# Performance work log

Hardware: AMD Instinct MI355X
Metric: run time of the kernel (lower is better)

## Reference

```python
import jax, jax.numpy as jnp
import numpy as np

B, T, D_IN, D, N = 8, 1024, 512, 512, 64

def setup_inputs() -> dict:
    key = jax.random.key(0)
    ks = jax.random.split(key, 8)
    s = 0.02  # weight init scale keeps tanh/softmax in sane range
    return {
        'x': jax.random.normal(ks[0], (B, T, D_IN), jnp.float32),
        'h_tape_init': jax.random.normal(ks[1], (B, N, D), jnp.float32),
        'h_work_init': jax.random.normal(ks[2], (B, D), jnp.float32) * 0.1,
        'W_h': jax.random.normal(ks[3], (D, D), jnp.float32) * s,
        'W_xz': jax.random.normal(ks[4], (2 * D, D_IN), jnp.float32) * s,
        'b_h': jnp.zeros((D,), jnp.float32),
        'W_write': jax.random.normal(ks[5], (D, D), jnp.float32) * s,
        'g_z': jnp.ones((D,), jnp.float32),
        'g_r': jnp.ones((D,), jnp.float32),
        'g_h': jnp.ones((D,), jnp.float32),
        'b_gate': jnp.zeros((D,), jnp.float32),
    }

def reference(x, h_tape_init, h_work_init, W_h, W_xz, b_h, W_write, g_z, g_r, g_h, b_gate):
    d = W_h.shape[0]
    scale = 1.0 / np.sqrt(d).astype(np.float32)
    xz = jnp.einsum('btk,ek->bte', x, W_xz)          # [B,T,2D]
    x_proj = xz[..., :d]
    z = xz[..., d:]

    def step(carry, inp):
        h_tape, h_work = carry                        # [B,N,D], [B,D]
        x_t, z_t = inp                                # [B,D], [B,D]
        read_scores = jnp.einsum('bd,bnd->bn', h_work, h_tape) * scale
        read_attn = jax.nn.softmax(read_scores, axis=-1)
        read_val = jnp.einsum('bn,bnd->bd', read_attn, h_tape)
        h_new = jnp.tanh(x_t + h_work @ W_h.T + read_val + b_h)
        write_val = h_new @ W_write.T
        write_scores = jnp.einsum('bd,bnd->bn', write_val, h_tape) * scale
        write_attn = jax.nn.softmax(write_scores, axis=-1)[..., None]  # [B,N,1]
        h_tape_new = h_tape * (1.0 - write_attn) + write_val[:, None, :] * write_attn
        gate_in = jnp.clip(z_t * g_z + read_val * g_r + h_new * g_h + b_gate, -20.0, 20.0)
        out = h_new * jax.nn.silu(gate_in)
        return (h_tape_new, h_new), out

    (h_tape_final, _), outs = jax.lax.scan(
        step, (h_tape_init, h_work_init),
        (jnp.swapaxes(x_proj, 0, 1), jnp.swapaxes(z, 0, 1)))
    return jnp.swapaxes(outs, 0, 1), h_tape_final
```

## Files before the change

### kernel.cpp

```cpp
#include <hip/hip_runtime.h>
#include <math.h>

#define TT 1024
#define DD 512

typedef unsigned int u32;
typedef unsigned long long u64;
typedef _Float16 half2_t __attribute__((ext_vector_type(2)));

static __device__ __forceinline__ u64 aload64(const u64* p) {
    return __hip_atomic_load(p, __ATOMIC_RELAXED, __HIP_MEMORY_SCOPE_AGENT);
}
static __device__ __forceinline__ void astore64(u64* p, u64 v) {
    __hip_atomic_store(p, v, __ATOMIC_RELAXED, __HIP_MEMORY_SCOPE_AGENT);
}
static __device__ __forceinline__ u32 pkh2(float lo, float hi) {
    return __builtin_bit_cast(u32, __builtin_amdgcn_cvt_pkrtz(lo, hi));
}
static __device__ __forceinline__ float2 uph2(u32 v) {
    half2_t h = __builtin_bit_cast(half2_t, v);
    return make_float2((float)h.x, (float)h.y);
}
static __device__ __forceinline__ u64 mkword(u32 pay, u32 tag) {
    return ((u64)tag << 32) | (u64)pay;
}

static __device__ __forceinline__ float redux8(float v) {
    v += __shfl_xor(v, 1); v += __shfl_xor(v, 2); v += __shfl_xor(v, 4); return v;
}
static __device__ __forceinline__ float sum64(float v) {
    #pragma unroll
    for (int o = 32; o > 0; o >>= 1) v += __shfl_xor(v, o);
    return v;
}
static __device__ __forceinline__ float expc(float x) { return __expf(fminf(x, 60.f)); }
static __device__ __forceinline__ float fast_tanh(float x) {
    float xc = fminf(fmaxf(x, -15.f), 15.f);
    float e = __expf(2.f * xc);
    return (e - 1.f) / (e + 1.f);
}

__global__ __launch_bounds__(256) void proj_kernel(const float* __restrict__ x,
                                                   const float* __restrict__ Wxz,
                                                   float* __restrict__ xp,
                                                   float* __restrict__ z) {
    __shared__ float As[16][66];
    __shared__ float Bs[16][66];
    const int m0 = blockIdx.x * 64;
    const int n0 = blockIdx.y * 64;
    const int tid = threadIdx.x;
    const int tm = tid / 16, tn = tid % 16;
    float c[4][4] = {};
    for (int k0 = 0; k0 < 512; k0 += 16) {
        const int r = tid >> 2, c4 = (tid & 3) * 4;
        float4 a4 = *(const float4*)(x + (size_t)(m0 + r) * 512 + k0 + c4);
        float4 b4 = *(const float4*)(Wxz + (size_t)(n0 + r) * 512 + k0 + c4);
        As[c4 + 0][r] = a4.x; As[c4 + 1][r] = a4.y; As[c4 + 2][r] = a4.z; As[c4 + 3][r] = a4.w;
        Bs[c4 + 0][r] = b4.x; Bs[c4 + 1][r] = b4.y; Bs[c4 + 2][r] = b4.z; Bs[c4 + 3][r] = b4.w;
        __syncthreads();
        #pragma unroll
        for (int k = 0; k < 16; ++k) {
            float a0 = As[k][tm * 4 + 0], a1 = As[k][tm * 4 + 1];
            float a2 = As[k][tm * 4 + 2], a3 = As[k][tm * 4 + 3];
            float b0 = Bs[k][tn * 4 + 0], b1 = Bs[k][tn * 4 + 1];
            float b2 = Bs[k][tn * 4 + 2], b3 = Bs[k][tn * 4 + 3];
            c[0][0] += a0 * b0; c[0][1] += a0 * b1; c[0][2] += a0 * b2; c[0][3] += a0 * b3;
            c[1][0] += a1 * b0; c[1][1] += a1 * b1; c[1][2] += a1 * b2; c[1][3] += a1 * b3;
            c[2][0] += a2 * b0; c[2][1] += a2 * b1; c[2][2] += a2 * b2; c[2][3] += a2 * b3;
            c[3][0] += a3 * b0; c[3][1] += a3 * b1; c[3][2] += a3 * b2; c[3][3] += a3 * b3;
        }
        __syncthreads();
    }
    #pragma unroll
    for (int i = 0; i < 4; ++i) {
        const int m = m0 + tm * 4 + i;
        #pragma unroll
        for (int j = 0; j < 4; ++j) {
            const int e = n0 + tn * 4 + j;
            if (e < 512) xp[(size_t)m * 512 + e] = c[i][j];
            else         z[(size_t)m * 512 + (e - 512)] = c[i][j];
        }
    }
}

__global__ __launch_bounds__(512) void rec_kernel(
    const float* __restrict__ tape0, const float* __restrict__ hwork0,
    const float* __restrict__ W_h, const float* __restrict__ b_h,
    const float* __restrict__ W_write,
    const float* __restrict__ g_z, const float* __restrict__ g_r,
    const float* __restrict__ g_h, const float* __restrict__ b_gate,
    const float* __restrict__ Zbuf,
    float* __restrict__ out, float* __restrict__ tape_out,
    u64* hA, u64* cA) {
    __shared__ __align__(16) float tp[64][512];
    __shared__ __align__(16) float hw2[8][68];
    __shared__ __align__(16) float wvp[8][68];
    __shared__ float red[8][64];
    __shared__ __align__(16) float hnc[64];
    __shared__ float rvc[64], xpc[64], zc[64];
    __shared__ float a_l[64], c1_l[64], hhc[64], ws_l[64], q0_l[64];
    __shared__ float c2_s;

    const int b = blockIdx.x & 7, s = blockIdx.x >> 3;
    const int tid = threadIdx.x, lane = tid & 63, wid = tid >> 6;
    const int nrow = tid >> 3, l = tid & 7;
    const int sw = ((l ^ nrow) & 7) << 2;
    const int d0 = s * 64;
    const float scale = 0.044194173824159216f;

    float4 wh[16];
    float4 wwc[16];
    {
        const float4* w1 = (const float4*)(W_h + (size_t)(d0 + nrow) * DD + l * 64);
        #pragma unroll
        for (int j = 0; j < 16; ++j) wh[j] = w1[j];
        const float4* w2 = (const float4*)(W_write + (size_t)tid * DD + d0);
        #pragma unroll
        for (int j = 0; j < 16; ++j) wwc[j] = w2[j];
    }
    float bhr = 0.f, gz = 0.f, gr = 0.f, gh = 0.f, bg = 0.f;
    if (wid == 0) bhr = b_h[d0 + lane];
    if (wid == 1) { gz = g_z[d0 + lane]; gr = g_r[d0 + lane]; gh = g_h[d0 + lane]; bg = b_gate[d0 + lane]; }

    {
        const float* src = tape0 + (size_t)(b * 64 + nrow) * DD;
        #pragma unroll
        for (int i = 0; i < 16; ++i) {
            float4 v = *(const float4*)(src + l * 64 + 4 * i);
            *(float4*)&tp[nrow][(l * 64 + 4 * i) ^ sw] = v;
        }
    }
    hw2[tid >> 6][tid & 63] = hwork0[(size_t)b * DD + tid];
    {
        float* pw = &wvp[0][0];
        for (int i = tid; i < 8 * 68; i += 512) pw[i] = 0.f;
    }
    if (tid < 64) a_l[tid] = 0.f;
    if (tid == 0) c2_s = 0.f;
    float xpr = 0.f, zr = 0.f;
    if (wid == 2)      xpr = out[((size_t)(b * TT)) * DD + d0 + lane];
    else if (wid == 3) zr  = Zbuf[((size_t)(b * TT)) * DD + d0 + lane];
    __syncthreads();

    {
        float q0 = 0.f, hh = 0.f;
        #pragma unroll
        for (int i = 0; i < 16; ++i) {
            float4 t4 = *(const float4*)&tp[nrow][(l * 64 + 4 * i) ^ sw];
            float4 h4 = *(const float4*)&hw2[l][4 * i];
            q0 += t4.x * h4.x + t4.y * h4.y + t4.z * h4.z + t4.w * h4.w;
            hh += wh[i].x * h4.x + wh[i].y * h4.y + wh[i].z * h4.z + wh[i].w * h4.w;
        }
        q0 = redux8(q0); hh = redux8(hh);
        if (l == 0) { q0_l[nrow] = q0; hhc[nrow] = hh; }
    }
    __syncthreads();
    if (wid == 0) {
        float er = expc(scale * q0_l[lane]);
        float Zr = sum64(er);
        c1_l[lane] = __fdividef(er, Zr);
    }
    __syncthreads();

    for (int t = 0; t < TT; ++t) {
        const int p = t & 1;
        const u32 tg = (u32)(t + 1);

        if (wid == 2)      xpc[lane] = xpr;
        else if (wid == 3) zc[lane] = zr;
        {
            float acc = 0.f;
            #pragma unroll
            for (int k = 0; k < 8; ++k)
                acc += c1_l[wid * 8 + k] * tp[wid * 8 + k][(d0 + lane) ^ (((s ^ k) & 7) << 2)];
            red[wid][lane] = acc;
        }
        __syncthreads();
        if (wid == 0) {
            float rv = c2_s * wvp[s][lane];
            #pragma unroll
            for (int w = 0; w < 8; ++w) rv += red[w][lane];
            rvc[lane] = rv;
            hnc[lane] = fast_tanh(xpc[lane] + hhc[lane] + rv + bhr);
        }
        __syncthreads();
        if (wid == 0 && !(lane & 1))
            astore64(&hA[((size_t)p * 8 + b) * 256 + s * 32 + (lane >> 1)],
                     mkword(pkh2(hnc[lane], hnc[lane + 1]), tg));
        {
            float cj = 0.f;
            #pragma unroll
            for (int j = 0; j < 16; ++j) {
                float4 h4 = *(const float4*)&hnc[4 * j];
                cj += wwc[j].x * h4.x + wwc[j].y * h4.y + wwc[j].z * h4.z + wwc[j].w * h4.w;
            }
            float cn = __shfl_xor(cj, 1);
            if (!(tid & 1))
                astore64(&cA[(((size_t)p * 8 + b) * 8 + s) * 256 + (tid >> 1)],
                         mkword(pkh2(cj, cn), tg));
        }
        if (wid == 1) {
            float h = hnc[lane];
            float g = zc[lane] * gz + rvc[lane] * gr + h * gh + bg;
            g = fminf(fmaxf(g, -20.f), 20.f);
            float sig = 1.f / (1.f + __expf(-g));
            out[((size_t)(b * TT + t)) * DD + d0 + lane] = h * g * sig;
        }
        const float an = a_l[nrow];
        #pragma unroll
        for (int i = 0; i < 8; ++i) {
            const int c = (l * 64 + 4 * i) ^ sw;
            float4 t4 = *(const float4*)&tp[nrow][c];
            float4 w4 = *(const float4*)&wvp[l][4 * i];
            t4.x += an * (w4.x - t4.x); t4.y += an * (w4.y - t4.y);
            t4.z += an * (w4.z - t4.z); t4.w += an * (w4.w - t4.w);
            *(float4*)&tp[nrow][c] = t4;
        }
        u64 v0 = 0, v1 = 0, v2 = 0, v3 = 0, v4 = 0, v5 = 0, v6 = 0, v7 = 0, vhw = 0;
        if (tid < 256) {
            const u64* cb = cA + (((size_t)p * 8 + b) * 8) * 256 + tid;
            v0 = aload64(cb + 0 * 256); v1 = aload64(cb + 1 * 256);
            v2 = aload64(cb + 2 * 256); v3 = aload64(cb + 3 * 256);
            v4 = aload64(cb + 4 * 256); v5 = aload64(cb + 5 * 256);
            v6 = aload64(cb + 6 * 256); v7 = aload64(cb + 7 * 256);
        } else {
            vhw = aload64(hA + ((size_t)p * 8 + b) * 256 + (tid - 256));
        }
        #pragma unroll
        for (int i = 8; i < 16; ++i) {
            const int c = (l * 64 + 4 * i) ^ sw;
            float4 t4 = *(const float4*)&tp[nrow][c];
            float4 w4 = *(const float4*)&wvp[l][4 * i];
            t4.x += an * (w4.x - t4.x); t4.y += an * (w4.y - t4.y);
            t4.z += an * (w4.z - t4.z); t4.w += an * (w4.w - t4.w);
            *(float4*)&tp[nrow][c] = t4;
        }
        __syncthreads();
        if (tid < 256) {
            const u64* cb = cA + (((size_t)p * 8 + b) * 8) * 256 + tid;
            for (;;) {
                u32 m = 0;
                if ((u32)(v0 >> 32) == tg) m |= 1u;   if ((u32)(v1 >> 32) == tg) m |= 2u;
                if ((u32)(v2 >> 32) == tg) m |= 4u;   if ((u32)(v3 >> 32) == tg) m |= 8u;
                if ((u32)(v4 >> 32) == tg) m |= 16u;  if ((u32)(v5 >> 32) == tg) m |= 32u;
                if ((u32)(v6 >> 32) == tg) m |= 64u;  if ((u32)(v7 >> 32) == tg) m |= 128u;
                if (m == 0xffu) break;
                __builtin_amdgcn_s_sleep(1);
                if (!(m & 1u))   v0 = aload64(cb + 0 * 256);
                if (!(m & 2u))   v1 = aload64(cb + 1 * 256);
                if (!(m & 4u))   v2 = aload64(cb + 2 * 256);
                if (!(m & 8u))   v3 = aload64(cb + 3 * 256);
                if (!(m & 16u))  v4 = aload64(cb + 4 * 256);
                if (!(m & 32u))  v5 = aload64(cb + 5 * 256);
                if (!(m & 64u))  v6 = aload64(cb + 6 * 256);
                if (!(m & 128u)) v7 = aload64(cb + 7 * 256);
            }
            float lo = 0.f, hi = 0.f; float2 f;
            f = uph2((u32)v0); lo += f.x; hi += f.y;
            f = uph2((u32)v1); lo += f.x; hi += f.y;
            f = uph2((u32)v2); lo += f.x; hi += f.y;
            f = uph2((u32)v3); lo += f.x; hi += f.y;
            f = uph2((u32)v4); lo += f.x; hi += f.y;
            f = uph2((u32)v5); lo += f.x; hi += f.y;
            f = uph2((u32)v6); lo += f.x; hi += f.y;
            f = uph2((u32)v7); lo += f.x; hi += f.y;
            wvp[tid >> 5][2 * (tid & 31)]     = lo;
            wvp[tid >> 5][2 * (tid & 31) + 1] = hi;
        } else {
            const int k = tid - 256;
            const u64* hb = hA + ((size_t)p * 8 + b) * 256 + k;
            for (;;) {
                if ((u32)(vhw >> 32) == tg) break;
                __builtin_amdgcn_s_sleep(1);
                vhw = aload64(hb);
            }
            float2 hp = uph2((u32)vhw);
            hw2[k >> 5][2 * (k & 31)]     = hp.x;
            hw2[k >> 5][2 * (k & 31) + 1] = hp.y;
        }
        __syncthreads();
        float hwv = 0.f;
        {
            float ws = 0.f, q0 = 0.f, hh = 0.f;
            #pragma unroll
            for (int i = 0; i < 16; ++i) {
                float4 t4 = *(const float4*)&tp[nrow][(l * 64 + 4 * i) ^ sw];
                float4 w4 = *(const float4*)&wvp[l][4 * i];
                float4 h4 = *(const float4*)&hw2[l][4 * i];
                ws += w4.x * t4.x + w4.y * t4.y + w4.z * t4.z + w4.w * t4.w;
                q0 += h4.x * t4.x + h4.y * t4.y + h4.z * t4.z + h4.w * t4.w;
                hh += wh[i].x * h4.x + wh[i].y * h4.y + wh[i].z * h4.z + wh[i].w * h4.w;
            }
            ws = redux8(ws); q0 = redux8(q0); hh = redux8(hh);
            if (l == 0) { ws_l[nrow] = ws; q0_l[nrow] = q0; hhc[nrow] = hh; }
        }
        if (wid == 0) {
            const int r8 = lane >> 3, c8 = (lane & 7) * 8;
            float a = 0.f;
            #pragma unroll
            for (int k = 0; k < 8; ++k) a += hw2[r8][c8 + k] * wvp[r8][c8 + k];
            hwv = sum64(a);
        }
        if (wid == 2 && t + 1 < TT)      xpr = out[((size_t)(b * TT + t + 1)) * DD + d0 + lane];
        else if (wid == 3 && t + 1 < TT) zr  = Zbuf[((size_t)(b * TT + t + 1)) * DD + d0 + lane];
        __syncthreads();
        if (wid == 0) {
            float ew = expc(scale * ws_l[lane]);
            float Zw = sum64(ew);
            float a = __fdividef(ew, Zw);
            float q = (1.f - a) * q0_l[lane] + a * hwv;
            float er = expc(scale * q);
            float Zr = sum64(er);
            float r = __fdividef(er, Zr);
            a_l[lane] = a;
            c1_l[lane] = r * (1.f - a);
            float c2 = sum64(r * a);
            if (lane == 0) c2_s = c2;
        }
        __syncthreads();
    }

    {
        const float an = a_l[nrow];
        const int esw = ((s ^ nrow) & 7) << 2;
        float* dst = tape_out + ((size_t)(b * 64 + nrow)) * DD;
        #pragma unroll
        for (int i = 0; i < 2; ++i) {
            const int c0 = d0 + l * 8 + 4 * i;
            float4 t4 = *(const float4*)&tp[nrow][c0 ^ esw];
            float4 w4 = *(const float4*)&wvp[s][l * 8 + 4 * i];
            t4.x += an * (w4.x - t4.x); t4.y += an * (w4.y - t4.y);
            t4.z += an * (w4.z - t4.z); t4.w += an * (w4.w - t4.w);
            *(float4*)(dst + c0) = t4;
        }
    }
}

extern "C" void kernel_launch(void* const* d_in, const int* in_sizes, int n_in,
                              void* d_out, int out_size, void* d_ws, size_t ws_size,
                              hipStream_t stream) {
    const float* x       = (const float*)d_in[0];
    const float* tape0   = (const float*)d_in[1];
    const float* hwork0  = (const float*)d_in[2];
    const float* W_h     = (const float*)d_in[3];
    const float* W_xz    = (const float*)d_in[4];
    const float* b_h     = (const float*)d_in[5];
    const float* W_write = (const float*)d_in[6];
    const float* g_z     = (const float*)d_in[7];
    const float* g_r     = (const float*)d_in[8];
    const float* g_h     = (const float*)d_in[9];
    const float* b_gate  = (const float*)d_in[10];

    float* out  = (float*)d_out;
    float* tout = out + (size_t)8 * TT * DD;

    char* ws = (char*)d_ws;
    u64* hA   = (u64*)ws;
    u64* cA   = (u64*)(ws + 32768);
    float* Zbuf = (float*)(ws + 393216);

    (void)in_sizes; (void)n_in; (void)out_size; (void)ws_size;

    dim3 pgrid(128, 16);
    proj_kernel<<<pgrid, 256, 0, stream>>>(x, W_xz, out, Zbuf);
    rec_kernel<<<64, 512, 0, stream>>>(tape0, hwork0, W_h, b_h, W_write,
                                       g_z, g_r, g_h, b_gate, Zbuf,
                                       out, tout, hA, cA);
}
```

Baseline: 4.977 ms.

## Cut per-step barriers by fusing read_val/tanh into softmax warp and double-buffering write values

Moves the read-value reduction and tanh into wave 0 right after the softmax, so h_new is ready at the end of each step and two block barriers per timestep disappear. The write-value buffer is double-buffered by step parity so the tape update can run before the new write values are published without a separate barrier, and updated tape rows are kept in registers for the following score dot products instead of being re-read from LDS. The trade-off is that a single wave now does the 64-row read_val loop serially, which lengthens the critical path and raises register pressure (launch bounds also ask for two blocks per CU).

```diff
diff --git a/kernel.cpp b/kernel.cpp
--- a/kernel.cpp
+++ b/kernel.cpp
@@ -83,7 +83,7 @@
     }
 }
 
-__global__ __launch_bounds__(512) void rec_kernel(
+__global__ __launch_bounds__(512, 2) void rec_kernel(
     const float* __restrict__ tape0, const float* __restrict__ hwork0,
     const float* __restrict__ W_h, const float* __restrict__ b_h,
     const float* __restrict__ W_write,
@@ -94,12 +94,12 @@
     u64* hA, u64* cA) {
     __shared__ __align__(16) float tp[64][512];
     __shared__ __align__(16) float hw2[8][68];
-    __shared__ __align__(16) float wvp[8][68];
-    __shared__ float red[8][64];
+    __shared__ __align__(16) float wvp[2][8][68];
     __shared__ __align__(16) float hnc[64];
-    __shared__ float rvc[64], xpc[64], zc[64];
-    __shared__ float a_l[64], c1_l[64], hhc[64], ws_l[64], q0_l[64];
-    __shared__ float c2_s;
+    __shared__ float rvc[64];
+    __shared__ float a_l[64], c1_l[64];
+    __shared__ float ws_l[64], q0_l[64], hhc[64];
+    __shared__ float hwv_s;
 
     const int b = blockIdx.x & 7, s = blockIdx.x >> 3;
     const int tid = threadIdx.x, lane = tid & 63, wid = tid >> 6;
@@ -132,14 +132,13 @@
     }
     hw2[tid >> 6][tid & 63] = hwork0[(size_t)b * DD + tid];
     {
-        float* pw = &wvp[0][0];
-        for (int i = tid; i < 8 * 68; i += 512) pw[i] = 0.f;
+        float* pw = &wvp[0][0][0];
+        for (int i = tid; i < 2 * 8 * 68; i += 512) pw[i] = 0.f;
     }
     if (tid < 64) a_l[tid] = 0.f;
-    if (tid == 0) c2_s = 0.f;
-    float xpr = 0.f, zr = 0.f;
-    if (wid == 2)      xpr = out[((size_t)(b * TT)) * DD + d0 + lane];
-    else if (wid == 3) zr  = Zbuf[((size_t)(b * TT)) * DD + d0 + lane];
+    float xpr = 0.f, zr = 0.f, hr = 0.f;
+    if (wid == 0)      xpr = out[((size_t)(b * TT)) * DD + d0 + lane];
+    else if (wid == 1) zr  = Zbuf[((size_t)(b * TT)) * DD + d0 + lane];
     __syncthreads();
 
     {
@@ -158,7 +157,14 @@
     if (wid == 0) {
         float er = expc(scale * q0_l[lane]);
         float Zr = sum64(er);
-        c1_l[lane] = __fdividef(er, Zr);
+        float r = __fdividef(er, Zr);
+        c1_l[lane] = r;
+        float rv = 0.f;
+        #pragma unroll 8
+        for (int n = 0; n < 64; ++n)
+            rv += c1_l[n] * tp[n][(d0 + lane) ^ (((s ^ n) & 7) << 2)];
+        float h = fast_tanh(xpr + hhc[lane] + rv + bhr);
+        hr = h; hnc[lane] = h; rvc[lane] = rv;
     }
     __syncthreads();
 
@@ -166,27 +172,12 @@
         const int p = t & 1;
         const u32 tg = (u32)(t + 1);
 
-        if (wid == 2)      xpc[lane] = xpr;
-        else if (wid == 3) zc[lane] = zr;
-        {
-            float acc = 0.f;
-            #pragma unroll
-            for (int k = 0; k < 8; ++k)
-                acc += c1_l[wid * 8 + k] * tp[wid * 8 + k][(d0 + lane) ^ (((s ^ k) & 7) << 2)];
-            red[wid][lane] = acc;
-        }
-        __syncthreads();
         if (wid == 0) {
-            float rv = c2_s * wvp[s][lane];
-            #pragma unroll
-            for (int w = 0; w < 8; ++w) rv += red[w][lane];
-            rvc[lane] = rv;
-            hnc[lane] = fast_tanh(xpc[lane] + hhc[lane] + rv + bhr);
-        }
-        __syncthreads();
-        if (wid == 0 && !(lane & 1))
-            astore64(&hA[((size_t)p * 8 + b) * 256 + s * 32 + (lane >> 1)],
-                     mkword(pkh2(hnc[lane], hnc[lane + 1]), tg));
+            float hn = __shfl_xor(hr, 1);
+            if (!(lane & 1))
+                astore64(&hA[((size_t)p * 8 + b) * 256 + s * 32 + (lane >> 1)],
+                         mkword(pkh2(hr, hn), tg));
+        }
         {
             float cj = 0.f;
             #pragma unroll
@@ -201,43 +192,33 @@
         }
         if (wid == 1) {
             float h = hnc[lane];
-            float g = zc[lane] * gz + rvc[lane] * gr + h * gh + bg;
+            float g = zr * gz + rvc[lane] * gr + h * gh + bg;
             g = fminf(fmaxf(g, -20.f), 20.f);
             float sig = 1.f / (1.f + __expf(-g));
             out[((size_t)(b * TT + t)) * DD + d0 + lane] = h * g * sig;
-        }
+            if (t + 1 < TT) zr = Zbuf[((size_t)(b * TT + t + 1)) * DD + d0 + lane];
+        }
+        if (wid == 0 && t + 1 < TT) xpr = out[((size_t)(b * TT + t + 1)) * DD + d0 + lane];
+
         const float an = a_l[nrow];
-        #pragma unroll
-        for (int i = 0; i < 8; ++i) {
+        float4 t4[16];
+        #pragma unroll
+        for (int i = 0; i < 16; ++i) {
             const int c = (l * 64 + 4 * i) ^ sw;
-            float4 t4 = *(const float4*)&tp[nrow][c];
-            float4 w4 = *(const float4*)&wvp[l][4 * i];
-            t4.x += an * (w4.x - t4.x); t4.y += an * (w4.y - t4.y);
-            t4.z += an * (w4.z - t4.z); t4.w += an * (w4.w - t4.w);
-            *(float4*)&tp[nrow][c] = t4;
-        }
-        u64 v0 = 0, v1 = 0, v2 = 0, v3 = 0, v4 = 0, v5 = 0, v6 = 0, v7 = 0, vhw = 0;
+            float4 v = *(const float4*)&tp[nrow][c];
+            float4 w4 = *(const float4*)&wvp[1 - p][l][4 * i];
+            v.x += an * (w4.x - v.x); v.y += an * (w4.y - v.y);
+            v.z += an * (w4.z - v.z); v.w += an * (w4.w - v.w);
+            *(float4*)&tp[nrow][c] = v;
+            t4[i] = v;
+        }
+
         if (tid < 256) {
             const u64* cb = cA + (((size_t)p * 8 + b) * 8) * 256 + tid;
-            v0 = aload64(cb + 0 * 256); v1 = aload64(cb + 1 * 256);
-            v2 = aload64(cb + 2 * 256); v3 = aload64(cb + 3 * 256);
-            v4 = aload64(cb + 4 * 256); v5 = aload64(cb + 5 * 256);
-            v6 = aload64(cb + 6 * 256); v7 = aload64(cb + 7 * 256);
-        } else {
-            vhw = aload64(hA + ((size_t)p * 8 + b) * 256 + (tid - 256));
-        }
-        #pragma unroll
-        for (int i = 8; i < 16; ++i) {
-            const int c = (l * 64 + 4 * i) ^ sw;
-            float4 t4 = *(const float4*)&tp[nrow][c];
-            float4 w4 = *(const float4*)&wvp[l][4 * i];
-            t4.x += an * (w4.x - t4.x); t4.y += an * (w4.y - t4.y);
-            t4.z += an * (w4.z - t4.z); t4.w += an * (w4.w - t4.w);
-            *(float4*)&tp[nrow][c] = t4;
-        }
-        __syncthreads();
-        if (tid < 256) {
-            const u64* cb = cA + (((size_t)p * 8 + b) * 8) * 256 + tid;
+            u64 v0 = aload64(cb + 0 * 256), v1 = aload64(cb + 1 * 256);
+            u64 v2 = aload64(cb + 2 * 256), v3 = aload64(cb + 3 * 256);
+            u64 v4 = aload64(cb + 4 * 256), v5 = aload64(cb + 5 * 256);
+            u64 v6 = aload64(cb + 6 * 256), v7 = aload64(cb + 7 * 256);
             for (;;) {
                 u32 m = 0;
                 if ((u32)(v0 >> 32) == tg) m |= 1u;   if ((u32)(v1 >> 32) == tg) m |= 2u;
@@ -264,58 +245,64 @@
             f = uph2((u32)v5); lo += f.x; hi += f.y;
             f = uph2((u32)v6); lo += f.x; hi += f.y;
             f = uph2((u32)v7); lo += f.x; hi += f.y;
-            wvp[tid >> 5][2 * (tid & 31)]     = lo;
-            wvp[tid >> 5][2 * (tid & 31) + 1] = hi;
+            wvp[p][tid >> 5][2 * (tid & 31)]     = lo;
+            wvp[p][tid >> 5][2 * (tid & 31) + 1] = hi;
         } else {
             const int k = tid - 256;
             const u64* hb = hA + ((size_t)p * 8 + b) * 256 + k;
+            u64 v = aload64(hb);
             for (;;) {
-                if ((u32)(vhw >> 32) == tg) break;
+                if ((u32)(v >> 32) == tg) break;
                 __builtin_amdgcn_s_sleep(1);
-                vhw = aload64(hb);
+                v = aload64(hb);
             }
-            float2 hp = uph2((u32)vhw);
+            float2 hp = uph2((u32)v);
             hw2[k >> 5][2 * (k & 31)]     = hp.x;
             hw2[k >> 5][2 * (k & 31) + 1] = hp.y;
         }
         __syncthreads();
-        float hwv = 0.f;
+
         {
             float ws = 0.f, q0 = 0.f, hh = 0.f;
             #pragma unroll
             for (int i = 0; i < 16; ++i) {
-                float4 t4 = *(const float4*)&tp[nrow][(l * 64 + 4 * i) ^ sw];
-                float4 w4 = *(const float4*)&wvp[l][4 * i];
+                float4 w4 = *(const float4*)&wvp[p][l][4 * i];
                 float4 h4 = *(const float4*)&hw2[l][4 * i];
-                ws += w4.x * t4.x + w4.y * t4.y + w4.z * t4.z + w4.w * t4.w;
-                q0 += h4.x * t4.x + h4.y * t4.y + h4.z * t4.z + h4.w * t4.w;
+                ws += w4.x * t4[i].x + w4.y * t4[i].y + w4.z * t4[i].z + w4.w * t4[i].w;
+                q0 += h4.x * t4[i].x + h4.y * t4[i].y + h4.z * t4[i].z + h4.w * t4[i].w;
                 hh += wh[i].x * h4.x + wh[i].y * h4.y + wh[i].z * h4.z + wh[i].w * h4.w;
             }
             ws = redux8(ws); q0 = redux8(q0); hh = redux8(hh);
             if (l == 0) { ws_l[nrow] = ws; q0_l[nrow] = q0; hhc[nrow] = hh; }
         }
-        if (wid == 0) {
+        if (wid == 1) {
             const int r8 = lane >> 3, c8 = (lane & 7) * 8;
-            float a = 0.f;
+            float acc = 0.f;
             #pragma unroll
-            for (int k = 0; k < 8; ++k) a += hw2[r8][c8 + k] * wvp[r8][c8 + k];
-            hwv = sum64(a);
-        }
-        if (wid == 2 && t + 1 < TT)      xpr = out[((size_t)(b * TT + t + 1)) * DD + d0 + lane];
-        else if (wid == 3 && t + 1 < TT) zr  = Zbuf[((size_t)(b * TT + t + 1)) * DD + d0 + lane];
-        __syncthreads();
+            for (int k = 0; k < 8; ++k) acc += hw2[r8][c8 + k] * wvp[p][r8][c8 + k];
+            acc = sum64(acc);
+            if (lane == 0) hwv_s = acc;
+        }
+        __syncthreads();
+
         if (wid == 0) {
             float ew = expc(scale * ws_l[lane]);
             float Zw = sum64(ew);
             float a = __fdividef(ew, Zw);
-            float q = (1.f - a) * q0_l[lane] + a * hwv;
+            float q = (1.f - a) * q0_l[lane] + a * hwv_s;
             float er = expc(scale * q);
             float Zr = sum64(er);
             float r = __fdividef(er, Zr);
             a_l[lane] = a;
-            c1_l[lane] = r * (1.f - a);
+            float c1 = r * (1.f - a);
+            c1_l[lane] = c1;
             float c2 = sum64(r * a);
-            if (lane == 0) c2_s = c2;
+            float rv = c2 * wvp[p][s][lane];
+            #pragma unroll 8
+            for (int n = 0; n < 64; ++n)
+                rv += c1_l[n] * tp[n][(d0 + lane) ^ (((s ^ n) & 7) << 2)];
+            float h = fast_tanh(xpr + hhc[lane] + rv + bhr);
+            hr = h; hnc[lane] = h; rvc[lane] = rv;
         }
         __syncthreads();
     }
@@ -328,7 +315,7 @@
         for (int i = 0; i < 2; ++i) {
             const int c0 = d0 + l * 8 + 4 * i;
             float4 t4 = *(const float4*)&tp[nrow][c0 ^ esw];
-            float4 w4 = *(const float4*)&wvp[s][l * 8 + 4 * i];
+            float4 w4 = *(const float4*)&wvp[1][s][l * 8 + 4 * i];
             t4.x += an * (w4.x - t4.x); t4.y += an * (w4.y - t4.y);
             t4.z += an * (w4.z - t4.z); t4.w += an * (w4.w - t4.w);
             *(float4*)(dst + c0) = t4;
```

Measured after the change: 7.398 ms. +48.6%, slower.

## Add sc0 mirror buffers with transposed layout for vectorized cross-block polling

Applied to the files above, without the earlier changes.

Each published h/c word is now also written to a second buffer with sc0 cache-policy stores. The c-buffer is transposed so that each thread's 8 slices sit contiguously and can be fetched with four dwordx4 loads instead of eight scattered 64-bit atomic loads. Polling reads the mirror and falls back to the agent-scope atomic buffer every 16 iterations. The wvp tape-write buffer is double-buffered by step parity, and the hwv reduction moves to warp 1 and is passed through shared memory. This relies on inline asm cache-bit semantics for cross-CU visibility, which is a correctness risk, and doubles the global stores per step.

```diff
diff --git a/kernel.cpp b/kernel.cpp
--- a/kernel.cpp
+++ b/kernel.cpp
@@ -7,6 +7,7 @@
 typedef unsigned int u32;
 typedef unsigned long long u64;
 typedef _Float16 half2_t __attribute__((ext_vector_type(2)));
+typedef unsigned long long u64x2 __attribute__((ext_vector_type(2)));
 
 static __device__ __forceinline__ u64 aload64(const u64* p) {
     return __hip_atomic_load(p, __ATOMIC_RELAXED, __HIP_MEMORY_SCOPE_AGENT);
@@ -14,6 +15,16 @@
 static __device__ __forceinline__ void astore64(u64* p, u64 v) {
     __hip_atomic_store(p, v, __ATOMIC_RELAXED, __HIP_MEMORY_SCOPE_AGENT);
 }
+static __device__ __forceinline__ u64 lload64(const u64* p) {
+    u64 v;
+    asm volatile("global_load_dwordx2 %0, %1, off sc0\n\ts_waitcnt vmcnt(0)"
+                 : "=&v"(v) : "v"(p) : "memory");
+    return v;
+}
+static __device__ __forceinline__ void lstore64(u64* p, u64 v) {
+    asm volatile("global_store_dwordx2 %0, %1, off sc0" :: "v"(p), "v"(v) : "memory");
+}
+
 static __device__ __forceinline__ u32 pkh2(float lo, float hi) {
     return __builtin_bit_cast(u32, __builtin_amdgcn_cvt_pkrtz(lo, hi));
 }
@@ -91,14 +102,15 @@
     const float* __restrict__ g_h, const float* __restrict__ b_gate,
     const float* __restrict__ Zbuf,
     float* __restrict__ out, float* __restrict__ tape_out,
-    u64* hA, u64* cA) {
+    u64* hA, u64* cA, u64* hF, u64* cF) {
     __shared__ __align__(16) float tp[64][512];
     __shared__ __align__(16) float hw2[8][68];
-    __shared__ __align__(16) float wvp[8][68];
+    __shared__ __align__(16) float wvp[2][8][68];
     __shared__ float red[8][64];
     __shared__ __align__(16) float hnc[64];
     __shared__ float rvc[64], xpc[64], zc[64];
     __shared__ float a_l[64], c1_l[64], hhc[64], ws_l[64], q0_l[64];
+    __shared__ float hwv_s;
     __shared__ float c2_s;
 
     const int b = blockIdx.x & 7, s = blockIdx.x >> 3;
@@ -132,8 +144,8 @@
     }
     hw2[tid >> 6][tid & 63] = hwork0[(size_t)b * DD + tid];
     {
-        float* pw = &wvp[0][0];
-        for (int i = tid; i < 8 * 68; i += 512) pw[i] = 0.f;
+        float* pw = &wvp[0][0][0];
+        for (int i = tid; i < 2 * 8 * 68; i += 512) pw[i] = 0.f;
     }
     if (tid < 64) a_l[tid] = 0.f;
     if (tid == 0) c2_s = 0.f;
@@ -165,6 +177,7 @@
     for (int t = 0; t < TT; ++t) {
         const int p = t & 1;
         const u32 tg = (u32)(t + 1);
+        const size_t p8b = (size_t)p * 8 + b;
 
         if (wid == 2)      xpc[lane] = xpr;
         else if (wid == 3) zc[lane] = zr;
@@ -177,16 +190,19 @@
         }
         __syncthreads();
         if (wid == 0) {
-            float rv = c2_s * wvp[s][lane];
+            float rv = c2_s * wvp[1 - p][s][lane];
             #pragma unroll
             for (int w = 0; w < 8; ++w) rv += red[w][lane];
             rvc[lane] = rv;
             hnc[lane] = fast_tanh(xpc[lane] + hhc[lane] + rv + bhr);
         }
         __syncthreads();
-        if (wid == 0 && !(lane & 1))
-            astore64(&hA[((size_t)p * 8 + b) * 256 + s * 32 + (lane >> 1)],
-                     mkword(pkh2(hnc[lane], hnc[lane + 1]), tg));
+        if (wid == 0 && !(lane & 1)) {
+            u64 w = mkword(pkh2(hnc[lane], hnc[lane + 1]), tg);
+            const size_t idx = p8b * 256 + s * 32 + (lane >> 1);
+            lstore64(&hF[idx], w);
+            astore64(&hA[idx], w);
+        }
         {
             float cj = 0.f;
             #pragma unroll
@@ -195,9 +211,12 @@
                 cj += wwc[j].x * h4.x + wwc[j].y * h4.y + wwc[j].z * h4.z + wwc[j].w * h4.w;
             }
             float cn = __shfl_xor(cj, 1);
-            if (!(tid & 1))
-                astore64(&cA[(((size_t)p * 8 + b) * 8 + s) * 256 + (tid >> 1)],
-                         mkword(pkh2(cj, cn), tg));
+            if (!(tid & 1)) {
+                u64 w = mkword(pkh2(cj, cn), tg);
+                const size_t idx = (p8b * 256 + (size_t)(tid >> 1)) * 8 + s;
+                lstore64(&cF[idx], w);
+                astore64(&cA[idx], w);
+            }
         }
         if (wid == 1) {
             float h = hnc[lane];
@@ -211,34 +230,45 @@
         for (int i = 0; i < 8; ++i) {
             const int c = (l * 64 + 4 * i) ^ sw;
             float4 t4 = *(const float4*)&tp[nrow][c];
-            float4 w4 = *(const float4*)&wvp[l][4 * i];
+            float4 w4 = *(const float4*)&wvp[1 - p][l][4 * i];
             t4.x += an * (w4.x - t4.x); t4.y += an * (w4.y - t4.y);
             t4.z += an * (w4.z - t4.z); t4.w += an * (w4.w - t4.w);
             *(float4*)&tp[nrow][c] = t4;
         }
-        u64 v0 = 0, v1 = 0, v2 = 0, v3 = 0, v4 = 0, v5 = 0, v6 = 0, v7 = 0, vhw = 0;
+        u64x2 a0{}, a1{}, a2{}, a3{};
+        u64 vhw = 0;
+        const u64* cf = cF + (p8b * 256 + (size_t)tid) * 8;
+        const u64* ca = cA + (p8b * 256 + (size_t)tid) * 8;
+        const u64* hf = hF + p8b * 256 + (size_t)(tid & 255);
+        const u64* hb = hA + p8b * 256 + (size_t)(tid & 255);
         if (tid < 256) {
-            const u64* cb = cA + (((size_t)p * 8 + b) * 8) * 256 + tid;
-            v0 = aload64(cb + 0 * 256); v1 = aload64(cb + 1 * 256);
-            v2 = aload64(cb + 2 * 256); v3 = aload64(cb + 3 * 256);
-            v4 = aload64(cb + 4 * 256); v5 = aload64(cb + 5 * 256);
-            v6 = aload64(cb + 6 * 256); v7 = aload64(cb + 7 * 256);
+            asm volatile(
+                "global_load_dwordx4 %0, %4, off sc0\n\t"
+                "global_load_dwordx4 %1, %4, off offset:16 sc0\n\t"
+                "global_load_dwordx4 %2, %4, off offset:32 sc0\n\t"
+                "global_load_dwordx4 %3, %4, off offset:48 sc0"
+                : "=&v"(a0), "=&v"(a1), "=&v"(a2), "=&v"(a3)
+                : "v"(cf) : "memory");
         } else {
-            vhw = aload64(hA + ((size_t)p * 8 + b) * 256 + (tid - 256));
+            asm volatile("global_load_dwordx2 %0, %1, off sc0"
+                         : "=&v"(vhw) : "v"(hf) : "memory");
         }
         #pragma unroll
         for (int i = 8; i < 16; ++i) {
             const int c = (l * 64 + 4 * i) ^ sw;
             float4 t4 = *(const float4*)&tp[nrow][c];
-            float4 w4 = *(const float4*)&wvp[l][4 * i];
+            float4 w4 = *(const float4*)&wvp[1 - p][l][4 * i];
             t4.x += an * (w4.x - t4.x); t4.y += an * (w4.y - t4.y);
             t4.z += an * (w4.z - t4.z); t4.w += an * (w4.w - t4.w);
             *(float4*)&tp[nrow][c] = t4;
         }
         __syncthreads();
         if (tid < 256) {
-            const u64* cb = cA + (((size_t)p * 8 + b) * 8) * 256 + tid;
-            for (;;) {
+            asm volatile("s_waitcnt vmcnt(0)"
+                         : "+v"(a0), "+v"(a1), "+v"(a2), "+v"(a3) :: "memory");
+            u64 v0 = a0.x, v1 = a0.y, v2 = a1.x, v3 = a1.y;
+            u64 v4 = a2.x, v5 = a2.y, v6 = a3.x, v7 = a3.y;
+            for (int it = 1; ; ++it) {
                 u32 m = 0;
                 if ((u32)(v0 >> 32) == tg) m |= 1u;   if ((u32)(v1 >> 32) == tg) m |= 2u;
                 if ((u32)(v2 >> 32) == tg) m |= 4u;   if ((u32)(v3 >> 32) == tg) m |= 8u;
@@ -246,14 +276,24 @@
                 if ((u32)(v6 >> 32) == tg) m |= 64u;  if ((u32)(v7 >> 32) == tg) m |= 128u;
                 if (m == 0xffu) break;
                 __builtin_amdgcn_s_sleep(1);
-                if (!(m & 1u))   v0 = aload64(cb + 0 * 256);
-                if (!(m & 2u))   v1 = aload64(cb + 1 * 256);
-                if (!(m & 4u))   v2 = aload64(cb + 2 * 256);
-                if (!(m & 8u))   v3 = aload64(cb + 3 * 256);
-                if (!(m & 16u))  v4 = aload64(cb + 4 * 256);
-                if (!(m & 32u))  v5 = aload64(cb + 5 * 256);
-                if (!(m & 64u))  v6 = aload64(cb + 6 * 256);
-                if (!(m & 128u)) v7 = aload64(cb + 7 * 256);
+                if ((it & 15) == 0) {
+                    v0 = aload64(ca + 0); v1 = aload64(ca + 1);
+                    v2 = aload64(ca + 2); v3 = aload64(ca + 3);
+                    v4 = aload64(ca + 4); v5 = aload64(ca + 5);
+                    v6 = aload64(ca + 6); v7 = aload64(ca + 7);
+                } else {
+                    asm volatile(
+                        "global_load_dwordx4 %0, %4, off sc0\n\t"
+                        "global_load_dwordx4 %1, %4, off offset:16 sc0\n\t"
+                        "global_load_dwordx4 %2, %4, off offset:32 sc0\n\t"
+                        "global_load_dwordx4 %3, %4, off offset:48 sc0"
+                        : "=&v"(a0), "=&v"(a1), "=&v"(a2), "=&v"(a3)
+                        : "v"(cf) : "memory");
+                    asm volatile("s_waitcnt vmcnt(0)"
+                                 : "+v"(a0), "+v"(a1), "+v"(a2), "+v"(a3) :: "memory");
+                    v0 = a0.x; v1 = a0.y; v2 = a1.x; v3 = a1.y;
+                    v4 = a2.x; v5 = a2.y; v6 = a3.x; v7 = a3.y;
+                }
             }
             float lo = 0.f, hi = 0.f; float2 f;
             f = uph2((u32)v0); lo += f.x; hi += f.y;
@@ -264,28 +304,27 @@
             f = uph2((u32)v5); lo += f.x; hi += f.y;
             f = uph2((u32)v6); lo += f.x; hi += f.y;
             f = uph2((u32)v7); lo += f.x; hi += f.y;
-            wvp[tid >> 5][2 * (tid & 31)]     = lo;
-            wvp[tid >> 5][2 * (tid & 31) + 1] = hi;
+            wvp[p][tid >> 5][2 * (tid & 31)]     = lo;
+            wvp[p][tid >> 5][2 * (tid & 31) + 1] = hi;
         } else {
             const int k = tid - 256;
-            const u64* hb = hA + ((size_t)p * 8 + b) * 256 + k;
-            for (;;) {
+            asm volatile("s_waitcnt vmcnt(0)" : "+v"(vhw) :: "memory");
+            for (int it = 1; ; ++it) {
                 if ((u32)(vhw >> 32) == tg) break;
                 __builtin_amdgcn_s_sleep(1);
-                vhw = aload64(hb);
+                vhw = ((it & 15) == 0) ? aload64(hb) : lload64(hf);
             }
             float2 hp = uph2((u32)vhw);
             hw2[k >> 5][2 * (k & 31)]     = hp.x;
             hw2[k >> 5][2 * (k & 31) + 1] = hp.y;
         }
         __syncthreads();
-        float hwv = 0.f;
         {
             float ws = 0.f, q0 = 0.f, hh = 0.f;
             #pragma unroll
             for (int i = 0; i < 16; ++i) {
                 float4 t4 = *(const float4*)&tp[nrow][(l * 64 + 4 * i) ^ sw];
-                float4 w4 = *(const float4*)&wvp[l][4 * i];
+                float4 w4 = *(const float4*)&wvp[p][l][4 * i];
                 float4 h4 = *(const float4*)&hw2[l][4 * i];
                 ws += w4.x * t4.x + w4.y * t4.y + w4.z * t4.z + w4.w * t4.w;
                 q0 += h4.x * t4.x + h4.y * t4.y + h4.z * t4.z + h4.w * t4.w;
@@ -294,12 +333,13 @@
             ws = redux8(ws); q0 = redux8(q0); hh = redux8(hh);
             if (l == 0) { ws_l[nrow] = ws; q0_l[nrow] = q0; hhc[nrow] = hh; }
         }
-        if (wid == 0) {
+        if (wid == 1) {
             const int r8 = lane >> 3, c8 = (lane & 7) * 8;
-            float a = 0.f;
+            float acc = 0.f;
             #pragma unroll
-            for (int k = 0; k < 8; ++k) a += hw2[r8][c8 + k] * wvp[r8][c8 + k];
-            hwv = sum64(a);
+            for (int k = 0; k < 8; ++k) acc += hw2[r8][c8 + k] * wvp[p][r8][c8 + k];
+            acc = sum64(acc);
+            if (lane == 0) hwv_s = acc;
         }
         if (wid == 2 && t + 1 < TT)      xpr = out[((size_t)(b * TT + t + 1)) * DD + d0 + lane];
         else if (wid == 3 && t + 1 < TT) zr  = Zbuf[((size_t)(b * TT + t + 1)) * DD + d0 + lane];
@@ -308,7 +348,7 @@
             float ew = expc(scale * ws_l[lane]);
             float Zw = sum64(ew);
             float a = __fdividef(ew, Zw);
-            float q = (1.f - a) * q0_l[lane] + a * hwv;
+            float q = (1.f - a) * q0_l[lane] + a * hwv_s;
             float er = expc(scale * q);
             float Zr = sum64(er);
             float r = __fdividef(er, Zr);
@@ -328,7 +368,7 @@
         for (int i = 0; i < 2; ++i) {
             const int c0 = d0 + l * 8 + 4 * i;
             float4 t4 = *(const float4*)&tp[nrow][c0 ^ esw];
-            float4 w4 = *(const float4*)&wvp[s][l * 8 + 4 * i];
+            float4 w4 = *(const float4*)&wvp[1][s][l * 8 + 4 * i];
             t4.x += an * (w4.x - t4.x); t4.y += an * (w4.y - t4.y);
             t4.z += an * (w4.z - t4.z); t4.w += an * (w4.w - t4.w);
             *(float4*)(dst + c0) = t4;
@@ -357,7 +397,9 @@
     char* ws = (char*)d_ws;
     u64* hA   = (u64*)ws;
     u64* cA   = (u64*)(ws + 32768);
-    float* Zbuf = (float*)(ws + 393216);
+    u64* hF   = (u64*)(ws + 294912);
+    u64* cF   = (u64*)(ws + 327680);
+    float* Zbuf = (float*)(ws + 593920);
 
     (void)in_sizes; (void)n_in; (void)out_size; (void)ws_size;
 
@@ -365,5 +407,5 @@
     proj_kernel<<<pgrid, 256, 0, stream>>>(x, W_xz, out, Zbuf);
     rec_kernel<<<64, 512, 0, stream>>>(tape0, hwork0, W_h, b_h, W_write,
                                        g_z, g_r, g_h, b_gate, Zbuf,
-                                       out, tout, hA, cA);
-}
+                                       out, tout, hA, cA, hF, cF);
+}
```

After: 8.342 ms. +67.6%, slower.
